# Performance work log

Hardware: AMD Instinct MI355X
Metric: run time of the kernel (lower is better)

Reference implementation:

```python
import jax, jax.numpy as jnp
import numpy as np

N = 16384           # nodes
E = 131072          # edges per graph (avg degree 16)
D_BODY = 2048
D_FACE = 512
H = 32              # hidden width (encoder / GCN)
BN_EPS = 1e-5


def _batchnorm(x, gamma, beta):
    # BatchNorm1d in training mode: biased batch stats over the node/batch dim
    mu = jnp.mean(x, axis=0)
    var = jnp.var(x, axis=0)
    return (x - mu) * jax.lax.rsqrt(var + BN_EPS) * gamma + beta


def _prelu(x, a):
    return jnp.where(x > 0, x, a * x)


def _gcn(x, feats, src, dst, W, b, n):
    # Edge weight = ReLU(cosine similarity of raw feats); GCN symmetric norm with self loops.
    fn = feats * jax.lax.rsqrt(jnp.sum(feats * feats, axis=1, keepdims=True) + 1e-12)
    sim = jax.nn.relu(jnp.sum(fn[src] * fn[dst], axis=1))        # [E]
    loop = jnp.arange(n)
    s = jnp.concatenate([src, loop])
    d = jnp.concatenate([dst, loop])
    w = jnp.concatenate([sim, jnp.ones((n,), x.dtype)])
    deg = jax.ops.segment_sum(w, d, num_segments=n)              # weighted in-degree
    dn = jax.lax.rsqrt(jnp.clip(deg, 1e-6))
    coef = dn[s] * dn[d] * w                                     # [E+N]
    agg = jax.ops.segment_sum(x[s] * coef[:, None], d, num_segments=n)  # [N,H]
    return agg @ W + b


def setup_inputs() -> dict:
    key = jax.random.key(0)
    ks = jax.random.split(key, 20)
    inp = {
        "x": jax.random.normal(ks[0], (N, 2), jnp.float32),
        "body_feats": jax.random.normal(ks[1], (N, D_BODY), jnp.float32),
        "face_feats": jax.random.normal(ks[2], (N, D_FACE), jnp.float32),
        "edge_index_body": jax.random.randint(ks[3], (2, E), 0, N),
        "edge_index_face": jax.random.randint(ks[4], (2, E), 0, N),
        # encoder: Linear(2,32) -> BN(32) -> PReLU -> Dropout(0) -> Linear(32,32)
        "enc_w1": jax.random.normal(ks[5], (2, H), jnp.float32) * 0.5,
        "enc_b1": jnp.zeros((H,), jnp.float32),
        "bn_gamma": jnp.ones((H,), jnp.float32),
        "bn_beta": jnp.zeros((H,), jnp.float32),
        "prelu_a": jnp.float32(0.25),
        "enc_w2": jax.random.normal(ks[6], (H, H), jnp.float32) * 0.18,
        "enc_b2": jnp.zeros((H,), jnp.float32),
        "w0_w": jax.random.normal(ks[7], (H, 1), jnp.float32) * 0.18,
        "w0_b": jnp.zeros((1,), jnp.float32),
        "gcnb_w": jax.random.normal(ks[8], (H, H), jnp.float32) * 0.18,
        "gcnb_b": jnp.zeros((H,), jnp.float32),
        "gcnf_w": jax.random.normal(ks[9], (H, H), jnp.float32) * 0.18,
        "gcnf_b": jnp.zeros((H,), jnp.float32),
        "wb_w": jax.random.normal(ks[10], (H, 1), jnp.float32) * 0.18,
        "wb_b": jnp.zeros((1,), jnp.float32),
        "wf_w": jax.random.normal(ks[11], (H, 1), jnp.float32) * 0.18,
        "wf_b": jnp.zeros((1,), jnp.float32),
    }
    return inp


def reference(x, body_feats, face_feats, edge_index_body, edge_index_face,
              enc_w1, enc_b1, bn_gamma, bn_beta, prelu_a, enc_w2, enc_b2,
              w0_w, w0_b, gcnb_w, gcnb_b, gcnf_w, gcnf_b, wb_w, wb_b, wf_w, wf_b):
    n = x.shape[0]
    h = _prelu(_batchnorm(x @ enc_w1 + enc_b1, bn_gamma, bn_beta), prelu_a)
    emb = h @ enc_w2 + enc_b2                                    # [N,32]
    xb = _gcn(emb, body_feats, edge_index_body[0], edge_index_body[1], gcnb_w, gcnb_b, n)
    xf = _gcn(emb, face_feats, edge_index_face[0], edge_index_face[1], gcnf_w, gcnf_b, n)
    lin = (emb @ w0_w + w0_b)[:, 0]
    sb = (xb @ wb_w + wb_b)[:, 0]
    sf = (xf @ wf_w + wf_b)[:, 0]
    return lin + sb + sf                                          # [N]
```

## Files before the change

kernel.cpp:

```cpp
#include <hip/hip_runtime.h>
#include <hip/hip_fp16.h>

#define N_NODES 16384
#define N_EDGES 131072
#define DB 2048
#define DF 512
#define FP8_SCALE 16.0f
#define FP8_DESCALE (1.0f / 256.0f)
#define SPREAD 16
#define BUCKET 64

#define WS_STATS   0
#define WS_PAR     320
#define WS_DNB     576
#define WS_DNF     (WS_DNB + N_NODES)
#define WS_WQB     (WS_DNF + N_NODES)
#define WS_WQF     (WS_WQB + N_NODES)
#define WS_CNTB    (WS_WQF + N_NODES)
#define WS_CNTF    (WS_CNTB + N_NODES * SPREAD)
#define WS_EDGEB   (WS_CNTF + N_NODES * SPREAD)
#define WS_EDGEF   (WS_EDGEB + N_NODES * BUCKET)
#define WS_FNB     (WS_EDGEF + N_NODES * BUCKET)
#define WS_FNF     (WS_FNB + N_NODES * DB / 4)

typedef float fv2 __attribute__((ext_vector_type(2)));

#if __has_builtin(__builtin_amdgcn_cvt_pk_f32_fp8) && __has_builtin(__builtin_amdgcn_cvt_pk_fp8_f32)
#define HAS_FP8HW 1
#else
#define HAS_FP8HW 0
#endif

__device__ __forceinline__ uint16_t f2h_bits(float f) {
    union { __half h; uint16_t u; } c; c.h = __float2half_rn(f); return c.u;
}
__device__ __forceinline__ float h_bits2f(uint16_t u) {
    union { uint16_t u; __half h; } c; c.u = u; return __half2float(c.h);
}

#if !HAS_FP8HW
__device__ __forceinline__ float fp8d_soft(uint32_t b) {
    uint32_t s = (b >> 7) & 1u, e = (b >> 3) & 0xFu, m = b & 7u;
    float v = (e == 0) ? (float)m * 0.001953125f
                       : (1.0f + (float)m * 0.125f) * exp2f((float)((int)e - 7));
    return s ? -v : v;
}
__device__ __forceinline__ uint32_t fp8e_soft(float f) {
    uint32_t s = (__float_as_uint(f) >> 31) << 7;
    float a = fabsf(f);
    if (a < 0.015625f) {
        int m = (int)rintf(a * 512.0f);
        if (m > 7) return s | (1u << 3);
        return s | (uint32_t)m;
    }
    uint32_t u = __float_as_uint(a);
    uint32_t r = u + 0x000FFFFFu + ((u >> 20) & 1u);
    int e8 = (int)(r >> 23) - 127 + 7;
    if (e8 >= 16) return s | (15u << 3) | 6u;
    return s | ((uint32_t)e8 << 3) | ((r >> 20) & 7u);
}
#endif

__device__ __forceinline__ float u32dot(uint32_t u, const float* s, float acc) {
#if HAS_FP8HW
    fv2 lo = __builtin_amdgcn_cvt_pk_f32_fp8(u, false);
    fv2 hi = __builtin_amdgcn_cvt_pk_f32_fp8(u, true);
    acc += s[0] * lo.x; acc += s[1] * lo.y;
    acc += s[2] * hi.x; acc += s[3] * hi.y;
#else
    acc += s[0] * fp8d_soft(u & 0xFF);
    acc += s[1] * fp8d_soft((u >> 8) & 0xFF);
    acc += s[2] * fp8d_soft((u >> 16) & 0xFF);
    acc += s[3] * fp8d_soft((u >> 24) & 0xFF);
#endif
    return acc;
}
__device__ __forceinline__ void u32cvt(uint32_t u, float* d) {
#if HAS_FP8HW
    fv2 lo = __builtin_amdgcn_cvt_pk_f32_fp8(u, false);
    fv2 hi = __builtin_amdgcn_cvt_pk_f32_fp8(u, true);
    d[0] = lo.x; d[1] = lo.y; d[2] = hi.x; d[3] = hi.y;
#else
    d[0] = fp8d_soft(u & 0xFF); d[1] = fp8d_soft((u >> 8) & 0xFF);
    d[2] = fp8d_soft((u >> 16) & 0xFF); d[3] = fp8d_soft((u >> 24) & 0xFF);
#endif
}
__device__ __forceinline__ uint32_t pack4_fp8(float a, float b, float c, float d) {
#if HAS_FP8HW
    uint32_t u = 0;
    u = __builtin_amdgcn_cvt_pk_fp8_f32(a, b, u, false);
    u = __builtin_amdgcn_cvt_pk_fp8_f32(c, d, u, true);
    return u;
#else
    return fp8e_soft(a) | (fp8e_soft(b) << 8) | (fp8e_soft(c) << 16) | (fp8e_soft(d) << 24);
#endif
}
__device__ __forceinline__ float dot16_fp8(uint4 r, const float* s, float acc) {
    acc = u32dot(r.x, s + 0, acc);  acc = u32dot(r.y, s + 4, acc);
    acc = u32dot(r.z, s + 8, acc);  acc = u32dot(r.w, s + 12, acc);
    return acc;
}

__global__ void k_pre(const float* __restrict__ x, const float* __restrict__ bfeat,
                      const float* __restrict__ ffeat, float* __restrict__ ws) {
    int b = blockIdx.x;
    if (b < 64) {
        __shared__ float red[4][5];
        float s0 = 0.f, s1 = 0.f, s2 = 0.f, s3 = 0.f, s4 = 0.f;
        for (int i = b * 256 + threadIdx.x; i < N_NODES; i += 64 * 256) {
            float2 v = ((const float2*)x)[i];
            s0 += v.x; s1 += v.y;
            s2 += v.x * v.x; s3 += v.y * v.y; s4 += v.x * v.y;
        }
        #pragma unroll
        for (int off = 32; off; off >>= 1) {
            s0 += __shfl_down(s0, off); s1 += __shfl_down(s1, off);
            s2 += __shfl_down(s2, off); s3 += __shfl_down(s3, off);
            s4 += __shfl_down(s4, off);
        }
        int w = threadIdx.x >> 6;
        if ((threadIdx.x & 63) == 0) {
            red[w][0] = s0; red[w][1] = s1; red[w][2] = s2; red[w][3] = s3; red[w][4] = s4;
        }
        __syncthreads();
        if (threadIdx.x < 5) {
            ws[WS_STATS + b * 5 + threadIdx.x] =
                red[0][threadIdx.x] + red[1][threadIdx.x] +
                red[2][threadIdx.x] + red[3][threadIdx.x];
        }
    } else if (b < 576) {
        int j = (b - 64) * 256 + threadIdx.x;
        ((int4*)(ws + WS_CNTB))[j] = make_int4(0, 0, 0, 0);
    } else if (b < 4672) {
        int row = (b - 576) * 4 + (threadIdx.x >> 6);
        int lane = threadIdx.x & 63;
        const float4* F = (const float4*)bfeat + (size_t)row * (DB / 4);
        float4 a[8];
        float aa = 0.f;
        #pragma unroll
        for (int k = 0; k < 8; k++) {
            a[k] = F[8 * lane + k];
            aa += a[k].x * a[k].x + a[k].y * a[k].y + a[k].z * a[k].z + a[k].w * a[k].w;
        }
        #pragma unroll
        for (int off = 32; off; off >>= 1) aa += __shfl_xor(aa, off);
        float inv = rsqrtf(aa + 1e-12f) * FP8_SCALE;
        uint4* O = (uint4*)(ws + WS_FNB) + (size_t)row * 128;
        uint4 o0, o1;
        o0.x = pack4_fp8(a[0].x * inv, a[0].y * inv, a[0].z * inv, a[0].w * inv);
        o0.y = pack4_fp8(a[1].x * inv, a[1].y * inv, a[1].z * inv, a[1].w * inv);
        o0.z = pack4_fp8(a[2].x * inv, a[2].y * inv, a[2].z * inv, a[2].w * inv);
        o0.w = pack4_fp8(a[3].x * inv, a[3].y * inv, a[3].z * inv, a[3].w * inv);
        o1.x = pack4_fp8(a[4].x * inv, a[4].y * inv, a[4].z * inv, a[4].w * inv);
        o1.y = pack4_fp8(a[5].x * inv, a[5].y * inv, a[5].z * inv, a[5].w * inv);
        o1.z = pack4_fp8(a[6].x * inv, a[6].y * inv, a[6].z * inv, a[6].w * inv);
        o1.w = pack4_fp8(a[7].x * inv, a[7].y * inv, a[7].z * inv, a[7].w * inv);
        O[2 * lane]     = o0;
        O[2 * lane + 1] = o1;
    } else {
        int idx = (b - 4672) * 4 + (threadIdx.x >> 6);
        int lane = threadIdx.x & 63;
        if (idx >= N_NODES) return;
        const float4* F = (const float4*)ffeat + (size_t)idx * (DF / 4);
        float4 a0 = F[2 * lane];
        float4 a1 = F[2 * lane + 1];
        float aa = a0.x * a0.x + a0.y * a0.y + a0.z * a0.z + a0.w * a0.w
                 + a1.x * a1.x + a1.y * a1.y + a1.z * a1.z + a1.w * a1.w;
        #pragma unroll
        for (int off = 32; off; off >>= 1) aa += __shfl_xor(aa, off);
        float inv = rsqrtf(aa + 1e-12f) * FP8_SCALE;
        uint2 o;
        o.x = pack4_fp8(a0.x * inv, a0.y * inv, a0.z * inv, a0.w * inv);
        o.y = pack4_fp8(a1.x * inv, a1.y * inv, a1.z * inv, a1.w * inv);
        ((uint2*)(ws + WS_FNF))[(size_t)idx * 64 + lane] = o;
    }
}

__global__ void k_scat(const int* __restrict__ eib, const int* __restrict__ eif,
                       const float* __restrict__ w1, const float* __restrict__ b1,
                       const float* __restrict__ gamma, const float* __restrict__ beta,
                       const float* __restrict__ w2, const float* __restrict__ b2,
                       const float* __restrict__ w0w, const float* __restrict__ w0b,
                       const float* __restrict__ gbw, const float* __restrict__ gbb,
                       const float* __restrict__ gfw, const float* __restrict__ gfb,
                       const float* __restrict__ wbw, const float* __restrict__ wbb,
                       const float* __restrict__ wfw, const float* __restrict__ wfb,
                       float* __restrict__ ws) {
    int b = blockIdx.x;
    if (b == 0) {
        __shared__ float st5[5];
        __shared__ float vb[32], vf[32];
        int t = threadIdx.x;
        if (t < 5) {
            float s = 0.f;
            for (int k = 0; k < 64; k++) s += ws[WS_STATS + k * 5 + t];
            st5[t] = s;
        }
        if (t >= 64 && t < 128) {
            int k = t & 31;
            const float* gw = (t < 96) ? gbw : gfw;
            const float* ww = (t < 96) ? wbw : wfw;
            float v = 0.f;
            for (int n = 0; n < 32; n++) v += gw[k * 32 + n] * ww[n];
            if (t < 96) vb[k] = v; else vf[k] = v;
        }
        __syncthreads();
        const float inv_n = 1.0f / (float)N_NODES;
        float m0 = st5[0] * inv_n, m1 = st5[1] * inv_n;
        float v0 = st5[2] * inv_n - m0 * m0;
        float v1 = st5[3] * inv_n - m1 * m1;
        float cv = st5[4] * inv_n - m0 * m1;
        float* par = ws + WS_PAR;
        int j = threadIdx.x;
        if (j < 32) {
            float W0 = w1[j], W1 = w1[32 + j];
            float mu  = m0 * W0 + m1 * W1 + b1[j];
            float var = W0 * W0 * v0 + W1 * W1 * v1 + 2.f * W0 * W1 * cv;
            float is  = rsqrtf(var + 1e-5f) * gamma[j];
            par[j]      = W0 * is;
            par[32 + j] = W1 * is;
            par[64 + j] = (b1[j] - mu) * is + beta[j];
            float u0 = 0.f, ub = 0.f, uf = 0.f;
            for (int k = 0; k < 32; k++) {
                float w2jk = w2[j * 32 + k];
                u0 += w2jk * w0w[k];
                ub += w2jk * vb[k];
                uf += w2jk * vf[k];
            }
            par[96 + j]  = u0;
            par[128 + j] = ub;
            par[160 + j] = uf;
        }
        if (threadIdx.x == 32) {
            float C = w0b[0] + wbb[0] + wfb[0];
            float pc0 = 0.f, pcb = 0.f, pcf = 0.f;
            for (int k = 0; k < 32; k++) {
                pc0 += b2[k] * w0w[k];
                pcb += b2[k] * vb[k];
                pcf += b2[k] * vf[k];
                C   += gbb[k] * wbw[k] + gfb[k] * wfw[k];
            }
            par[192] = C; par[193] = pc0; par[194] = pcb; par[195] = pcf;
        }
    } else {
        int e = (b - 1) * 256 + threadIdx.x;
        if (e < N_EDGES) {
            int s = eib[e], d = eib[N_EDGES + e];
            int pos = atomicAdd(&((int*)(ws + WS_CNTB))[d * SPREAD], 1);
            if (pos < BUCKET)
                ((uint32_t*)(ws + WS_EDGEB))[d * BUCKET + pos] = (uint32_t)s;
        } else {
            int e2 = e - N_EDGES;
            int s = eif[e2], d = eif[N_EDGES + e2];
            int pos = atomicAdd(&((int*)(ws + WS_CNTF))[d * SPREAD], 1);
            if (pos < BUCKET)
                ((uint32_t*)(ws + WS_EDGEF))[d * BUCKET + pos] = (uint32_t)s;
        }
    }
}

__device__ __forceinline__ float wave_p(const float* __restrict__ par, float2 v,
                                        float alpha, int coef_base, int lane) {
    int j = lane & 31;
    float z = v.x * par[j] + v.y * par[32 + j] + par[64 + j];
    float h = z > 0.f ? z : alpha * z;
    float p = h * par[coef_base + j];
    #pragma unroll
    for (int off = 16; off; off >>= 1) p += __shfl_xor(p, off);
    return p;
}

__global__ void k_edge_all(const float* __restrict__ x, const float* __restrict__ prelu_a,
                           float* __restrict__ ws) {
    int wid  = (int)((blockIdx.x * blockDim.x + threadIdx.x) >> 6);
    int lane = threadIdx.x & 63;
    const float* par = ws + WS_PAR;
    if (wid < N_NODES) {
        uint32_t* edges = (uint32_t*)(ws + WS_EDGEB) + wid * BUCKET;
        int cnt = ((const int*)(ws + WS_CNTB))[wid * SPREAD];
        int en = cnt < BUCKET ? cnt : BUCKET;
        float wdeg = 0.f;
        if (en > 0) {
            const uint4* fn = (const uint4*)(ws + WS_FNB);
            const uint4* Dp = fn + (size_t)wid * 128;
            uint4 r0 = Dp[lane], r1 = Dp[lane + 64];
            float dstf[32];
            u32cvt(r0.x, dstf + 0);  u32cvt(r0.y, dstf + 4);
            u32cvt(r0.z, dstf + 8);  u32cvt(r0.w, dstf + 12);
            u32cvt(r1.x, dstf + 16); u32cvt(r1.y, dstf + 20);
            u32cvt(r1.z, dstf + 24); u32cvt(r1.w, dstf + 28);
            int i = 0;
            for (; i + 3 < en; i += 4) {
                uint32_t w[4];
                uint4 lo[4], hi[4];
                #pragma unroll
                for (int k = 0; k < 4; k++) w[k] = edges[i + k];
                #pragma unroll
                for (int k = 0; k < 4; k++) {
                    const uint4* P = fn + (size_t)(w[k] & 0xFFFFu) * 128;
                    lo[k] = P[lane]; hi[k] = P[lane + 64];
                }
                float s[4];
                #pragma unroll
                for (int k = 0; k < 4; k++)
                    s[k] = dot16_fp8(hi[k], dstf + 16, dot16_fp8(lo[k], dstf, 0.f));
                #pragma unroll
                for (int off = 32; off; off >>= 1) {
                    #pragma unroll
                    for (int k = 0; k < 4; k++) s[k] += __shfl_xor(s[k], off);
                }
                if (lane == 0) {
                    #pragma unroll
                    for (int k = 0; k < 4; k++) {
                        float m = fmaxf(s[k], 0.f) * FP8_DESCALE;
                        edges[i + k] = (w[k] & 0xFFFFu) | ((uint32_t)f2h_bits(m) << 16);
                        wdeg += m;
                    }
                }
            }
            for (; i < en; i++) {
                uint32_t w0 = edges[i];
                const uint4* A = fn + (size_t)(w0 & 0xFFFFu) * 128;
                uint4 a0 = A[lane], a1 = A[lane + 64];
                float s0 = dot16_fp8(a1, dstf + 16, dot16_fp8(a0, dstf, 0.f));
                #pragma unroll
                for (int off = 32; off; off >>= 1) s0 += __shfl_xor(s0, off);
                if (lane == 0) {
                    float m0 = fmaxf(s0, 0.f) * FP8_DESCALE;
                    edges[i] = (w0 & 0xFFFFu) | ((uint32_t)f2h_bits(m0) << 16);
                    wdeg += m0;
                }
            }
        }
        float2 v = ((const float2*)x)[wid];
        float pb = wave_p(par, v, prelu_a[0], 128, lane);
        if (lane == 0) {
            float dn = rsqrtf(fmaxf(1.f + wdeg, 1e-6f));
            ws[WS_DNB + wid] = dn;
            ws[WS_WQB + wid] = dn * (par[194] + pb);
        }
    } else {
        int nid = wid - N_NODES;
        if (nid >= N_NODES) return;
        uint32_t* edges = (uint32_t*)(ws + WS_EDGEF) + nid * BUCKET;
        int cnt = ((const int*)(ws + WS_CNTF))[nid * SPREAD];
        int en = cnt < BUCKET ? cnt : BUCKET;
        float wdeg = 0.f;
        if (en > 0) {
            const uint2* fn = (const uint2*)(ws + WS_FNF);
            uint2 sv = fn[(size_t)nid * 64 + lane];
            float dstf[8];
            u32cvt(sv.x, dstf); u32cvt(sv.y, dstf + 4);
            int i = 0;
            for (; i + 3 < en; i += 4) {
                uint32_t w0 = edges[i], w1 = edges[i + 1], w2 = edges[i + 2], w3 = edges[i + 3];
                uint2 r0 = fn[(size_t)(w0 & 0xFFFFu) * 64 + lane];
                uint2 r1 = fn[(size_t)(w1 & 0xFFFFu) * 64 + lane];
                uint2 r2 = fn[(size_t)(w2 & 0xFFFFu) * 64 + lane];
                uint2 r3 = fn[(size_t)(w3 & 0xFFFFu) * 64 + lane];
                float c0 = u32dot(r0.y, dstf + 4, u32dot(r0.x, dstf, 0.f));
                float c1 = u32dot(r1.y, dstf + 4, u32dot(r1.x, dstf, 0.f));
                float c2 = u32dot(r2.y, dstf + 4, u32dot(r2.x, dstf, 0.f));
                float c3 = u32dot(r3.y, dstf + 4, u32dot(r3.x, dstf, 0.f));
                #pragma unroll
                for (int off = 32; off; off >>= 1) {
                    c0 += __shfl_xor(c0, off); c1 += __shfl_xor(c1, off);
                    c2 += __shfl_xor(c2, off); c3 += __shfl_xor(c3, off);
                }
                if (lane == 0) {
                    float m0 = fmaxf(c0, 0.f) * FP8_DESCALE;
                    float m1 = fmaxf(c1, 0.f) * FP8_DESCALE;
                    float m2 = fmaxf(c2, 0.f) * FP8_DESCALE;
                    float m3 = fmaxf(c3, 0.f) * FP8_DESCALE;
                    edges[i]     = (w0 & 0xFFFFu) | ((uint32_t)f2h_bits(m0) << 16);
                    edges[i + 1] = (w1 & 0xFFFFu) | ((uint32_t)f2h_bits(m1) << 16);
                    edges[i + 2] = (w2 & 0xFFFFu) | ((uint32_t)f2h_bits(m2) << 16);
                    edges[i + 3] = (w3 & 0xFFFFu) | ((uint32_t)f2h_bits(m3) << 16);
                    wdeg += m0 + m1 + m2 + m3;
                }
            }
            for (; i < en; i++) {
                uint32_t w0 = edges[i];
                uint2 r0 = fn[(size_t)(w0 & 0xFFFFu) * 64 + lane];
                float c0 = u32dot(r0.y, dstf + 4, u32dot(r0.x, dstf, 0.f));
                #pragma unroll
                for (int off = 32; off; off >>= 1) c0 += __shfl_xor(c0, off);
                if (lane == 0) {
                    float m0 = fmaxf(c0, 0.f) * FP8_DESCALE;
                    edges[i] = (w0 & 0xFFFFu) | ((uint32_t)f2h_bits(m0) << 16);
                    wdeg += m0;
                }
            }
        }
        float2 v = ((const float2*)x)[nid];
        float pf = wave_p(par, v, prelu_a[0], 160, lane);
        if (lane == 0) {
            float dn = rsqrtf(fmaxf(1.f + wdeg, 1e-6f));
            ws[WS_DNF + nid] = dn;
            ws[WS_WQF + nid] = dn * (par[195] + pf);
        }
    }
}

__global__ void k_out(const float* __restrict__ x, const float* __restrict__ prelu_a,
                      float* __restrict__ out, const float* __restrict__ ws) {
    int wid  = (int)((blockIdx.x * blockDim.x + threadIdx.x) >> 6);
    int lane = threadIdx.x & 63;
    if (wid >= N_NODES) return;
    const float* par = ws + WS_PAR;
    const uint32_t* egB = (const uint32_t*)(ws + WS_EDGEB) + wid * BUCKET;
    int cntB = ((const int*)(ws + WS_CNTB))[wid * SPREAD];
    int enB = cntB < BUCKET ? cntB : BUCKET;
    float sB = 0.f;
    for (int e = lane; e < enB; e += 64) {
        uint32_t w = egB[e];
        float sm = h_bits2f((uint16_t)(w >> 16));
        if (sm > 0.f) sB += sm * ws[WS_WQB + (w & 0xFFFFu)];
    }
    const uint32_t* egF = (const uint32_t*)(ws + WS_EDGEF) + wid * BUCKET;
    int cntF = ((const int*)(ws + WS_CNTF))[wid * SPREAD];
    int enF = cntF < BUCKET ? cntF : BUCKET;
    float sF = 0.f;
    for (int e = lane; e < enF; e += 64) {
        uint32_t w = egF[e];
        float sm = h_bits2f((uint16_t)(w >> 16));
        if (sm > 0.f) sF += sm * ws[WS_WQF + (w & 0xFFFFu)];
    }
    float2 v = ((const float2*)x)[wid];
    float alpha = prelu_a[0];
    int j = lane & 31;
    float z = v.x * par[j] + v.y * par[32 + j] + par[64 + j];
    float h = z > 0.f ? z : alpha * z;
    float t0 = h * par[96 + j], tb = h * par[128 + j], tf = h * par[160 + j];
    if (lane >= 32) { t0 = 0.f; tb = 0.f; tf = 0.f; }
    #pragma unroll
    for (int off = 32; off; off >>= 1) {
        sB += __shfl_xor(sB, off); sF += __shfl_xor(sF, off);
        t0 += __shfl_xor(t0, off); tb += __shfl_xor(tb, off);
        tf += __shfl_xor(tf, off);
    }
    if (lane == 0) {
        float dnb = ws[WS_DNB + wid];
        float dnf = ws[WS_DNF + wid];
        float p0  = par[192] + par[193] + t0;
        float pvb = par[194] + tb;
        float pvf = par[195] + tf;
        out[wid] = p0 + dnb * dnb * pvb + dnb * sB + dnf * dnf * pvf + dnf * sF;
    }
}

extern "C" void kernel_launch(void* const* d_in, const int* in_sizes, int n_in,
                              void* d_out, int out_size, void* d_ws, size_t ws_size,
                              hipStream_t stream) {
    const float* x     = (const float*)d_in[0];
    const float* bfeat = (const float*)d_in[1];
    const float* ffeat = (const float*)d_in[2];
    const int*   eib   = (const int*)d_in[3];
    const int*   eif   = (const int*)d_in[4];
    const float* w1    = (const float*)d_in[5];
    const float* b1    = (const float*)d_in[6];
    const float* gam   = (const float*)d_in[7];
    const float* bet   = (const float*)d_in[8];
    const float* pa    = (const float*)d_in[9];
    const float* w2    = (const float*)d_in[10];
    const float* b2    = (const float*)d_in[11];
    const float* w0w   = (const float*)d_in[12];
    const float* w0b   = (const float*)d_in[13];
    const float* gbw   = (const float*)d_in[14];
    const float* gbb   = (const float*)d_in[15];
    const float* gfw   = (const float*)d_in[16];
    const float* gfb   = (const float*)d_in[17];
    const float* wbw   = (const float*)d_in[18];
    const float* wbb   = (const float*)d_in[19];
    const float* wfw   = (const float*)d_in[20];
    const float* wfb   = (const float*)d_in[21];

    float* ws  = (float*)d_ws;
    float* out = (float*)d_out;

    k_pre<<<dim3(8768), dim3(256), 0, stream>>>(x, bfeat, ffeat, ws);
    k_scat<<<dim3(1025), dim3(256), 0, stream>>>(
        eib, eif, w1, b1, gam, bet, w2, b2, w0w, w0b,
        gbw, gbb, gfw, gfb, wbw, wbb, wfw, wfb, ws);
    k_edge_all<<<dim3(2 * N_NODES / 4), dim3(256), 0, stream>>>(x, pa, ws);
    k_out<<<dim3(N_NODES / 4), dim3(256), 0, stream>>>(x, pa, out, ws);
}
```

Measured before the change: 120.9 us.

## Move BN stats into scatter kernel, pair edges per thread, unroll edge gather by 8

The input-statistics reduction moves out of the preprocessing kernel and into block 0 of the scatter kernel, so one block now reduces all of x on its own instead of 64 blocks writing partial sums. The edge scatter loads two edges per thread through int2 loads, which halves the number of scatter blocks. The cosine-similarity loop in the edge kernel gains an 8-way unrolled stage ahead of the existing 4-way stage, putting more gathers in flight. The cost is a serialized stats reduction in a single block, which may lengthen the scatter kernel's critical path, plus higher register pressure from the 8-wide unroll.

```diff
diff --git a/kernel.cpp b/kernel.cpp
--- a/kernel.cpp
+++ b/kernel.cpp
@@ -101,38 +101,14 @@
     return acc;
 }
 
-__global__ void k_pre(const float* __restrict__ x, const float* __restrict__ bfeat,
-                      const float* __restrict__ ffeat, float* __restrict__ ws) {
+__global__ void k_pre(const float* __restrict__ bfeat, const float* __restrict__ ffeat,
+                      float* __restrict__ ws) {
     int b = blockIdx.x;
-    if (b < 64) {
-        __shared__ float red[4][5];
-        float s0 = 0.f, s1 = 0.f, s2 = 0.f, s3 = 0.f, s4 = 0.f;
-        for (int i = b * 256 + threadIdx.x; i < N_NODES; i += 64 * 256) {
-            float2 v = ((const float2*)x)[i];
-            s0 += v.x; s1 += v.y;
-            s2 += v.x * v.x; s3 += v.y * v.y; s4 += v.x * v.y;
-        }
-        #pragma unroll
-        for (int off = 32; off; off >>= 1) {
-            s0 += __shfl_down(s0, off); s1 += __shfl_down(s1, off);
-            s2 += __shfl_down(s2, off); s3 += __shfl_down(s3, off);
-            s4 += __shfl_down(s4, off);
-        }
-        int w = threadIdx.x >> 6;
-        if ((threadIdx.x & 63) == 0) {
-            red[w][0] = s0; red[w][1] = s1; red[w][2] = s2; red[w][3] = s3; red[w][4] = s4;
-        }
-        __syncthreads();
-        if (threadIdx.x < 5) {
-            ws[WS_STATS + b * 5 + threadIdx.x] =
-                red[0][threadIdx.x] + red[1][threadIdx.x] +
-                red[2][threadIdx.x] + red[3][threadIdx.x];
-        }
-    } else if (b < 576) {
-        int j = (b - 64) * 256 + threadIdx.x;
+    if (b < 512) {
+        int j = b * 256 + threadIdx.x;
         ((int4*)(ws + WS_CNTB))[j] = make_int4(0, 0, 0, 0);
-    } else if (b < 4672) {
-        int row = (b - 576) * 4 + (threadIdx.x >> 6);
+    } else if (b < 4608) {
+        int row = (b - 512) * 4 + (threadIdx.x >> 6);
         int lane = threadIdx.x & 63;
         const float4* F = (const float4*)bfeat + (size_t)row * (DB / 4);
         float4 a[8];
@@ -158,9 +134,8 @@
         O[2 * lane]     = o0;
         O[2 * lane + 1] = o1;
     } else {
-        int idx = (b - 4672) * 4 + (threadIdx.x >> 6);
+        int idx = (b - 4608) * 4 + (threadIdx.x >> 6);
         int lane = threadIdx.x & 63;
-        if (idx >= N_NODES) return;
         const float4* F = (const float4*)ffeat + (size_t)idx * (DF / 4);
         float4 a0 = F[2 * lane];
         float4 a1 = F[2 * lane + 1];
@@ -177,6 +152,7 @@
 }
 
 __global__ void k_scat(const int* __restrict__ eib, const int* __restrict__ eif,
+                       const float* __restrict__ x,
                        const float* __restrict__ w1, const float* __restrict__ b1,
                        const float* __restrict__ gamma, const float* __restrict__ beta,
                        const float* __restrict__ w2, const float* __restrict__ b2,
@@ -188,13 +164,25 @@
                        float* __restrict__ ws) {
     int b = blockIdx.x;
     if (b == 0) {
+        __shared__ float red[4][5];
         __shared__ float st5[5];
         __shared__ float vb[32], vf[32];
         int t = threadIdx.x;
-        if (t < 5) {
-            float s = 0.f;
-            for (int k = 0; k < 64; k++) s += ws[WS_STATS + k * 5 + t];
-            st5[t] = s;
+        float s0 = 0.f, s1 = 0.f, s2 = 0.f, s3 = 0.f, s4 = 0.f;
+        for (int i = t; i < N_NODES; i += 256) {
+            float2 v = ((const float2*)x)[i];
+            s0 += v.x; s1 += v.y;
+            s2 += v.x * v.x; s3 += v.y * v.y; s4 += v.x * v.y;
+        }
+        #pragma unroll
+        for (int off = 32; off; off >>= 1) {
+            s0 += __shfl_down(s0, off); s1 += __shfl_down(s1, off);
+            s2 += __shfl_down(s2, off); s3 += __shfl_down(s3, off);
+            s4 += __shfl_down(s4, off);
+        }
+        int w = t >> 6;
+        if ((t & 63) == 0) {
+            red[w][0] = s0; red[w][1] = s1; red[w][2] = s2; red[w][3] = s3; red[w][4] = s4;
         }
         if (t >= 64 && t < 128) {
             int k = t & 31;
@@ -205,13 +193,15 @@
             if (t < 96) vb[k] = v; else vf[k] = v;
         }
         __syncthreads();
+        if (t < 5) st5[t] = red[0][t] + red[1][t] + red[2][t] + red[3][t];
+        __syncthreads();
         const float inv_n = 1.0f / (float)N_NODES;
         float m0 = st5[0] * inv_n, m1 = st5[1] * inv_n;
         float v0 = st5[2] * inv_n - m0 * m0;
         float v1 = st5[3] * inv_n - m1 * m1;
         float cv = st5[4] * inv_n - m0 * m1;
         float* par = ws + WS_PAR;
-        int j = threadIdx.x;
+        int j = t;
         if (j < 32) {
             float W0 = w1[j], W1 = w1[32 + j];
             float mu  = m0 * W0 + m1 * W1 + b1[j];
@@ -231,7 +221,7 @@
             par[128 + j] = ub;
             par[160 + j] = uf;
         }
-        if (threadIdx.x == 32) {
+        if (t == 32) {
             float C = w0b[0] + wbb[0] + wfb[0];
             float pc0 = 0.f, pcb = 0.f, pcf = 0.f;
             for (int k = 0; k < 32; k++) {
@@ -243,18 +233,27 @@
             par[192] = C; par[193] = pc0; par[194] = pcb; par[195] = pcf;
         }
     } else {
-        int e = (b - 1) * 256 + threadIdx.x;
+        int p = (b - 1) * 256 + threadIdx.x;
+        int e = 2 * p;
         if (e < N_EDGES) {
-            int s = eib[e], d = eib[N_EDGES + e];
-            int pos = atomicAdd(&((int*)(ws + WS_CNTB))[d * SPREAD], 1);
-            if (pos < BUCKET)
-                ((uint32_t*)(ws + WS_EDGEB))[d * BUCKET + pos] = (uint32_t)s;
+            int2 sp = *(const int2*)(eib + e);
+            int2 dp = *(const int2*)(eib + N_EDGES + e);
+            int pos0 = atomicAdd(&((int*)(ws + WS_CNTB))[dp.x * SPREAD], 1);
+            if (pos0 < BUCKET)
+                ((uint32_t*)(ws + WS_EDGEB))[dp.x * BUCKET + pos0] = (uint32_t)sp.x;
+            int pos1 = atomicAdd(&((int*)(ws + WS_CNTB))[dp.y * SPREAD], 1);
+            if (pos1 < BUCKET)
+                ((uint32_t*)(ws + WS_EDGEB))[dp.y * BUCKET + pos1] = (uint32_t)sp.y;
         } else {
-            int e2 = e - N_EDGES;
-            int s = eif[e2], d = eif[N_EDGES + e2];
-            int pos = atomicAdd(&((int*)(ws + WS_CNTF))[d * SPREAD], 1);
-            if (pos < BUCKET)
-                ((uint32_t*)(ws + WS_EDGEF))[d * BUCKET + pos] = (uint32_t)s;
+            int q = e - N_EDGES;
+            int2 sp = *(const int2*)(eif + q);
+            int2 dp = *(const int2*)(eif + N_EDGES + q);
+            int pos0 = atomicAdd(&((int*)(ws + WS_CNTF))[dp.x * SPREAD], 1);
+            if (pos0 < BUCKET)
+                ((uint32_t*)(ws + WS_EDGEF))[dp.x * BUCKET + pos0] = (uint32_t)sp.x;
+            int pos1 = atomicAdd(&((int*)(ws + WS_CNTF))[dp.y * SPREAD], 1);
+            if (pos1 < BUCKET)
+                ((uint32_t*)(ws + WS_EDGEF))[dp.y * BUCKET + pos1] = (uint32_t)sp.y;
         }
     }
 }
@@ -290,6 +289,34 @@
             u32cvt(r1.x, dstf + 16); u32cvt(r1.y, dstf + 20);
             u32cvt(r1.z, dstf + 24); u32cvt(r1.w, dstf + 28);
             int i = 0;
+            for (; i + 7 < en; i += 8) {
+                uint32_t w[8];
+                uint4 lo[8], hi[8];
+                #pragma unroll
+                for (int k = 0; k < 8; k++) w[k] = edges[i + k];
+                #pragma unroll
+                for (int k = 0; k < 8; k++) {
+                    const uint4* P = fn + (size_t)(w[k] & 0xFFFFu) * 128;
+                    lo[k] = P[lane]; hi[k] = P[lane + 64];
+                }
+                float s[8];
+                #pragma unroll
+                for (int k = 0; k < 8; k++)
+                    s[k] = dot16_fp8(hi[k], dstf + 16, dot16_fp8(lo[k], dstf, 0.f));
+                #pragma unroll
+                for (int off = 32; off; off >>= 1) {
+                    #pragma unroll
+                    for (int k = 0; k < 8; k++) s[k] += __shfl_xor(s[k], off);
+                }
+                if (lane == 0) {
+                    #pragma unroll
+                    for (int k = 0; k < 8; k++) {
+                        float m = fmaxf(s[k], 0.f) * FP8_DESCALE;
+                        edges[i + k] = (w[k] & 0xFFFFu) | ((uint32_t)f2h_bits(m) << 16);
+                        wdeg += m;
+                    }
+                }
+            }
             for (; i + 3 < en; i += 4) {
                 uint32_t w[4];
                 uint4 lo[4], hi[4];
@@ -478,9 +505,9 @@
     float* ws  = (float*)d_ws;
     float* out = (float*)d_out;
 
-    k_pre<<<dim3(8768), dim3(256), 0, stream>>>(x, bfeat, ffeat, ws);
-    k_scat<<<dim3(1025), dim3(256), 0, stream>>>(
-        eib, eif, w1, b1, gam, bet, w2, b2, w0w, w0b,
+    k_pre<<<dim3(8704), dim3(256), 0, stream>>>(bfeat, ffeat, ws);
+    k_scat<<<dim3(513), dim3(256), 0, stream>>>(
+        eib, eif, x, w1, b1, gam, bet, w2, b2, w0w, w0b,
         gbw, gbb, gfw, gfb, wbw, wbb, wfw, wfb, ws);
     k_edge_all<<<dim3(2 * N_NODES / 4), dim3(256), 0, stream>>>(x, pa, ws);
     k_out<<<dim3(N_NODES / 4), dim3(256), 0, stream>>>(x, pa, out, ws);
```

New measurement: 142.8 us. +18.1%, slower.
